# Performance work log

Measured on AMD Instinct MI355X. Metric: run time of the kernel, lower is better.

The kernel has to match this reference:

```python
import jax, jax.numpy as jnp
import numpy as np

DIM = 256
H = 8
D = 64
G = 64
INNER = H * D
SCALE = D ** -0.5


def setup_inputs() -> dict:
    key = jax.random.key(0)
    ks = jax.random.split(key, 12)
    B, N = 4, 16384
    x = jax.random.normal(ks[0], (B, N, DIM), dtype=jnp.float32)
    s = lambda fan_in: 1.0 / np.sqrt(fan_in)
    W_fx = jax.random.normal(ks[1], (DIM, INNER), dtype=jnp.float32) * s(DIM)
    b_fx = jnp.zeros((INNER,), dtype=jnp.float32)
    W_x = jax.random.normal(ks[2], (DIM, INNER), dtype=jnp.float32) * s(DIM)
    b_x = jnp.zeros((INNER,), dtype=jnp.float32)
    # orthogonal-ish init for slice projection
    A = jax.random.normal(ks[3], (G, D), dtype=jnp.float32)
    Q, _ = jnp.linalg.qr(A.T)  # (D, G) with orthonormal columns
    W_slice = Q[:, :G].astype(jnp.float32)  # (D, G)
    b_slice = jnp.zeros((G,), dtype=jnp.float32)
    W_q = jax.random.normal(ks[4], (D, D), dtype=jnp.float32) * s(D)
    W_k = jax.random.normal(ks[5], (D, D), dtype=jnp.float32) * s(D)
    W_v = jax.random.normal(ks[6], (D, D), dtype=jnp.float32) * s(D)
    W_out = jax.random.normal(ks[7], (INNER, DIM), dtype=jnp.float32) * s(INNER)
    b_out = jnp.zeros((DIM,), dtype=jnp.float32)
    temperature = jnp.ones((1, H, 1, 1), dtype=jnp.float32) * 0.5
    return {"x": x, "W_fx": W_fx, "b_fx": b_fx, "W_x": W_x, "b_x": b_x,
            "W_slice": W_slice, "b_slice": b_slice, "W_q": W_q, "W_k": W_k,
            "W_v": W_v, "W_out": W_out, "b_out": b_out, "temperature": temperature}


def reference(x, W_fx, b_fx, W_x, b_x, W_slice, b_slice, W_q, W_k, W_v, W_out, b_out, temperature):
    B, N, _ = x.shape
    # per-head projections: (B, H, N, D)
    fx_mid = (x @ W_fx + b_fx).reshape(B, N, H, D).transpose(0, 2, 1, 3)
    x_mid = (x @ W_x + b_x).reshape(B, N, H, D).transpose(0, 2, 1, 3)
    temp = jnp.clip(temperature, 0.1, 5.0)  # (1, H, 1, 1)
    # soft dispatch weights over G slices: (B, H, N, G)
    slice_weights = jax.nn.softmax((x_mid @ W_slice + b_slice) / temp, axis=-1)
    slice_norm = slice_weights.sum(axis=2)  # (B, H, G)
    # dispatch: pool N nodes into G slice tokens
    slice_token = jnp.einsum('bhnc,bhng->bhgc', fx_mid, slice_weights)
    slice_token = slice_token / (slice_norm[..., None] + 1e-5)
    # small attention among G slice tokens
    q = slice_token @ W_q
    k = slice_token @ W_k
    v = slice_token @ W_v
    attn = jax.nn.softmax(jnp.einsum('bhgc,bhkc->bhgk', q, k) * SCALE, axis=-1)
    out_slice = jnp.einsum('bhgk,bhkc->bhgc', attn, v)
    # combine: scatter slice tokens back to nodes
    out_x = jnp.einsum('bhgc,bhng->bhnc', out_slice, slice_weights)
    out_x = out_x.transpose(0, 2, 1, 3).reshape(B, N, INNER)
    return out_x @ W_out + b_out
```

## Files before the change

### kernel.cpp

```cpp
#include <hip/hip_runtime.h>
#include <hip/hip_bf16.h>


#define B_ 4
#define N_ 16384
#define DIM_ 256
#define H_ 8
#define D_ 64
#define G_ 64
#define INNER_ 512
#define SCALE_ 0.125f

typedef __attribute__((ext_vector_type(8))) short bf16x8;
typedef __attribute__((ext_vector_type(4))) float f32x4;
typedef unsigned short ushort_t;

#define MFMA(a, b, c) __builtin_amdgcn_mfma_f32_16x16x32_bf16((a), (b), (c), 0, 0, 0)

__device__ __forceinline__ ushort_t f2bf(float f) {
  unsigned u = __builtin_bit_cast(unsigned, f);
  u += 0x7FFFu + ((u >> 16) & 1u);
  return (ushort_t)(u >> 16);
}
__device__ __forceinline__ float bf2f(ushort_t h) {
  return __builtin_bit_cast(float, ((unsigned)h) << 16);
}
__device__ __forceinline__ uint2 pack4(f32x4 v) {
  uint2 r;
  r.x = (unsigned)f2bf(v[0]) | ((unsigned)f2bf(v[1]) << 16);
  r.y = (unsigned)f2bf(v[2]) | ((unsigned)f2bf(v[3]) << 16);
  return r;
}
__device__ __forceinline__ void gload16(const ushort_t* gsrc, char* ldst) {
  __builtin_amdgcn_global_load_lds(
      (const __attribute__((address_space(1))) unsigned int*)gsrc,
      (__attribute__((address_space(3))) unsigned int*)ldst, 16, 0, 0);
}

__global__ __launch_bounds__(256) void k0_prep(
    const float* __restrict__ x, const float* __restrict__ Wfx,
    const float* __restrict__ Wout, ushort_t* __restrict__ xh,
    ushort_t* __restrict__ xl, ushort_t* __restrict__ wfxt,
    ushort_t* __restrict__ wot) {
  const int bid = blockIdx.x;
  const int t = threadIdx.x;
  if (bid < 2048) {
    const float4* x4 = (const float4*)x;
    const int base = bid * 256 + t;
#pragma unroll
    for (int i = 0; i < 8; ++i) {
      const int idx = base + i * 524288;
      const float4 v = x4[idx];
      ushort_t h0 = f2bf(v.x), h1 = f2bf(v.y), h2 = f2bf(v.z), h3 = f2bf(v.w);
      uint2 hp, lp;
      hp.x = (unsigned)h0 | ((unsigned)h1 << 16);
      hp.y = (unsigned)h2 | ((unsigned)h3 << 16);
      lp.x = (unsigned)f2bf(v.x - bf2f(h0)) | ((unsigned)f2bf(v.y - bf2f(h1)) << 16);
      lp.y = (unsigned)f2bf(v.z - bf2f(h2)) | ((unsigned)f2bf(v.w - bf2f(h3)) << 16);
      *(uint2*)&xh[(size_t)idx * 4] = hp;
      *(uint2*)&xl[(size_t)idx * 4] = lp;
    }
  } else if (bid < 2560) {
    const int f = (bid - 2048) * 256 + t;
    const int k = f & 255, c = (f >> 8) & 63, h = f >> 14;
    wfxt[f] = f2bf(Wfx[(size_t)k * INNER_ + h * 64 + c]);
  } else {
    const int idx = (bid - 2560) * 256 + t;
    const int c = idx & 63, d = (idx >> 6) & 255, h = idx >> 14;
    wot[idx] = f2bf(Wout[(size_t)(h * 64 + c) * DIM_ + d]);
  }
}

__global__ __launch_bounds__(256) void k0b_comb(
    const float* __restrict__ Wx, const float* __restrict__ Wsl,
    const float* __restrict__ bx, const float* __restrict__ bsl,
    ushort_t* __restrict__ wcth, ushort_t* __restrict__ wctl,
    float* __restrict__ lbias) {
  __shared__ float wsl_s[4096];
  __shared__ float wx_s[64 * 65];
  const int h = blockIdx.x;
  const int t = threadIdx.x;
#pragma unroll
  for (int i = 0; i < 16; ++i) wsl_s[i * 256 + t] = Wsl[i * 256 + t];
  __syncthreads();
  if (t < 64) {
    float a = bsl[t];
    for (int dd = 0; dd < 64; ++dd) a += bx[h * 64 + dd] * wsl_s[dd * 64 + t];
    lbias[h * 64 + t] = a;
  }
  const int g = t & 63, ko = t >> 6;
  for (int kc = 0; kc < 4; ++kc) {
    __syncthreads();
#pragma unroll
    for (int i = 0; i < 16; ++i) {
      const int f = i * 256 + t;
      wx_s[(f >> 6) * 65 + (f & 63)] =
          Wx[(size_t)(kc * 64 + (f >> 6)) * INNER_ + h * 64 + (f & 63)];
    }
    __syncthreads();
    for (int kk = ko * 16; kk < ko * 16 + 16; ++kk) {
      float a = 0.f;
#pragma unroll 8
      for (int dd = 0; dd < 64; ++dd) a += wx_s[kk * 65 + dd] * wsl_s[dd * 64 + g];
      const int k = kc * 64 + kk;
      const ushort_t hi = f2bf(a);
      wcth[(size_t)(h * 64 + g) * 256 + k] = hi;
      wctl[(size_t)(h * 64 + g) * 256 + k] = f2bf(a - bf2f(hi));
    }
  }
}

__global__ __launch_bounds__(512, 4) void k1_proj(
    const ushort_t* __restrict__ xh, const ushort_t* __restrict__ xl,
    const ushort_t* __restrict__ wfxt, const ushort_t* __restrict__ wcth,
    const ushort_t* __restrict__ wctl, const float* __restrict__ bfx,
    const float* __restrict__ lbias, const float* __restrict__ temperature,
    ushort_t* __restrict__ w_buf, float* __restrict__ tok,
    float* __restrict__ nrm) {
  __shared__ __align__(16) char lds[57344];
  ushort_t* fxT = (ushort_t*)lds;
  ushort_t* wT = (ushort_t*)(lds + 17408);

  const int t = threadIdx.x;
  const int l = t & 63, w = t >> 6;
  const int l15 = l & 15, l4 = l >> 4;
  const int bid = blockIdx.x;
  const int tile = bid & 127, h = (bid >> 7) & 7, b = bid >> 10;
  const int n0 = tile * 128;
  const int bh = b * H_ + h;

  const ushort_t* xhg = xh + (size_t)(b * N_ + n0) * 256;
  const ushort_t* xlg = xl + (size_t)(b * N_ + n0) * 256;
  const ushort_t* wfg = wfxt + h * 16384;
  const ushort_t* wchg = wcth + h * 16384;
  const ushort_t* wclg = wctl + h * 16384;

  const int srow = l >> 2;
  const int schunk = (l & 3) * 8;

  f32x4 afx[4], alg[4];
#pragma unroll
  for (int cf = 0; cf < 4; ++cf) {
    const float bf_ = bfx[h * 64 + cf * 16 + l15];
    afx[cf][0] = bf_; afx[cf][1] = bf_; afx[cf][2] = bf_; afx[cf][3] = bf_;
    const float lb_ = lbias[h * 64 + cf * 16 + l15];
    alg[cf][0] = lb_; alg[cf][1] = lb_; alg[cf][2] = lb_; alg[cf][3] = lb_;
  }

#define STAGE(cur, ks)                                                          \
  {                                                                             \
    const int k0_ = (ks) * 32;                                                  \
    char* sb_ = lds + (cur) * 28672;                                            \
    gload16(xhg + (size_t)(w * 16 + srow) * 256 + k0_ + schunk, sb_ + w * 1024);\
    gload16(xlg + (size_t)(w * 16 + srow) * 256 + k0_ + schunk,                 \
            sb_ + 8192 + w * 1024);                                             \
    if (w < 4) {                                                                \
      gload16(wfg + (size_t)(w * 16 + srow) * 256 + k0_ + schunk,               \
              sb_ + 16384 + w * 1024);                                          \
      gload16(wclg + (size_t)(w * 16 + srow) * 256 + k0_ + schunk,              \
              sb_ + 24576 + w * 1024);                                          \
    } else {                                                                    \
      gload16(wchg + (size_t)((w - 4) * 16 + srow) * 256 + k0_ + schunk,        \
              sb_ + 20480 + (w - 4) * 1024);                                    \
    }                                                                           \
  }

  STAGE(0, 0);
  __syncthreads();
  int cur = 0;
  for (int ks = 0; ks < 8; ++ks) {
    if (ks < 7) STAGE(cur ^ 1, ks + 1);
    const char* sb = lds + cur * 28672;
    const int aoff = ((w * 16 + l15) * 32 + l4 * 8) * 2;
    const bf16x8 aXH = *(const bf16x8*)(sb + aoff);
    const bf16x8 aXL = *(const bf16x8*)(sb + 8192 + aoff);
    const int boff = (l15 * 32 + l4 * 8) * 2;
#pragma unroll
    for (int cf = 0; cf < 4; ++cf) {
      const bf16x8 bWF = *(const bf16x8*)(sb + 16384 + cf * 1024 + boff);
      afx[cf] = MFMA(aXH, bWF, afx[cf]);
      const bf16x8 bCH = *(const bf16x8*)(sb + 20480 + cf * 1024 + boff);
      alg[cf] = MFMA(aXH, bCH, alg[cf]);
      alg[cf] = MFMA(aXL, bCH, alg[cf]);
      const bf16x8 bCL = *(const bf16x8*)(sb + 24576 + cf * 1024 + boff);
      alg[cf] = MFMA(aXH, bCL, alg[cf]);
    }
    __syncthreads();
    cur ^= 1;
  }
#undef STAGE

#pragma unroll
  for (int cf = 0; cf < 4; ++cf)
    *(uint2*)&fxT[(cf * 16 + l15) * 136 + w * 16 + l4 * 4] = pack4(afx[cf]);

  float tmp = temperature[h];
  tmp = fminf(fmaxf(tmp, 0.1f), 5.0f);
  const float itemp = 1.0f / tmp;
  float wv[4][4];
#pragma unroll
  for (int r = 0; r < 4; ++r) {
    float m = fmaxf(fmaxf(alg[0][r], alg[1][r]), fmaxf(alg[2][r], alg[3][r])) * itemp;
    m = fmaxf(m, __shfl_xor(m, 1));
    m = fmaxf(m, __shfl_xor(m, 2));
    m = fmaxf(m, __shfl_xor(m, 4));
    m = fmaxf(m, __shfl_xor(m, 8));
    float s = 0.f;
#pragma unroll
    for (int gf = 0; gf < 4; ++gf) {
      wv[r][gf] = __expf(alg[gf][r] * itemp - m);
      s += wv[r][gf];
    }
    s += __shfl_xor(s, 1);
    s += __shfl_xor(s, 2);
    s += __shfl_xor(s, 4);
    s += __shfl_xor(s, 8);
    const float inv = 1.0f / s;
#pragma unroll
    for (int gf = 0; gf < 4; ++gf) wv[r][gf] *= inv;
  }

#pragma unroll
  for (int gf = 0; gf < 4; ++gf) {
    float pn = wv[0][gf] + wv[1][gf] + wv[2][gf] + wv[3][gf];
    pn += __shfl_xor(pn, 16);
    pn += __shfl_xor(pn, 32);
    if (l4 == 0) atomicAdd(&nrm[bh * 64 + gf * 16 + l15], pn);
  }

#pragma unroll
  for (int gf = 0; gf < 4; ++gf) {
    f32x4 v;
    v[0] = wv[0][gf]; v[1] = wv[1][gf]; v[2] = wv[2][gf]; v[3] = wv[3][gf];
    *(uint2*)&wT[(gf * 16 + l15) * 136 + w * 16 + l4 * 4] = pack4(v);
  }
  __syncthreads();

  {
    const int n = t >> 2, q = t & 3;
    unsigned up[8];
#pragma unroll
    for (int j = 0; j < 8; ++j) {
      const unsigned e0 = wT[(q * 16 + 2 * j) * 136 + n];
      const unsigned e1 = wT[(q * 16 + 2 * j + 1) * 136 + n];
      up[j] = e0 | (e1 << 16);
    }
    ushort_t* wg = w_buf + ((size_t)bh * N_ + n0 + n) * 64 + q * 16;
    *(int4*)&wg[0] = *(int4*)&up[0];
    *(int4*)&wg[8] = *(int4*)&up[4];
  }

  f32x4 ap[2];
  ap[0] = (f32x4)0.f;
  ap[1] = (f32x4)0.f;
  const int gf0 = (w * 2) >> 2, cf0 = (w * 2) & 3;
  const int gf1 = (w * 2 + 1) >> 2, cf1 = (w * 2 + 1) & 3;
#pragma unroll
  for (int ks = 0; ks < 4; ++ks) {
    const bf16x8 aW0 = *(const bf16x8*)&wT[(gf0 * 16 + l15) * 136 + ks * 32 + l4 * 8];
    const bf16x8 bF0 = *(const bf16x8*)&fxT[(cf0 * 16 + l15) * 136 + ks * 32 + l4 * 8];
    ap[0] = MFMA(aW0, bF0, ap[0]);
    const bf16x8 aW1 = *(const bf16x8*)&wT[(gf1 * 16 + l15) * 136 + ks * 32 + l4 * 8];
    const bf16x8 bF1 = *(const bf16x8*)&fxT[(cf1 * 16 + l15) * 136 + ks * 32 + l4 * 8];
    ap[1] = MFMA(aW1, bF1, ap[1]);
  }
#pragma unroll
  for (int u = 0; u < 2; ++u) {
    const int gf = (w * 2 + u) >> 2, cf = (w * 2 + u) & 3;
    const int c = cf * 16 + l15;
#pragma unroll
    for (int r = 0; r < 4; ++r) {
      const int g = gf * 16 + l4 * 4 + r;
      atomicAdd(&tok[((size_t)bh * 64 + g) * 64 + c], ap[u][r]);
    }
  }
}

__global__ __launch_bounds__(256) void k2_attn(
    const float* __restrict__ tok, const float* __restrict__ nrm,
    const float* __restrict__ Wq, const float* __restrict__ Wk,
    const float* __restrict__ Wv, ushort_t* __restrict__ outST) {
  __shared__ float st[64 * 65];
  __shared__ float qs[64 * 65];
  __shared__ float ks[64 * 68];
  __shared__ float vs[64 * 68];
  const int t = threadIdx.x;
  const int g = t & 63, qd = t >> 6;
  const int bh = blockIdx.x;

  const float rn = 1.0f / (nrm[bh * 64 + g] + 1e-5f);
  const float* tkr = tok + (size_t)bh * 4096 + g * 64;
#pragma unroll
  for (int dd = 0; dd < 16; ++dd) {
    const int d = qd * 16 + dd;
    st[g * 65 + d] = tkr[d] * rn;
  }
  __syncthreads();

  float qa[16], ka[16], va[16];
#pragma unroll
  for (int dd = 0; dd < 16; ++dd) { qa[dd] = 0.f; ka[dd] = 0.f; va[dd] = 0.f; }
  for (int c = 0; c < 64; ++c) {
    const float s = st[g * 65 + c];
    const float* wqp = Wq + c * 64 + qd * 16;
    const float* wkp = Wk + c * 64 + qd * 16;
    const float* wvp = Wv + c * 64 + qd * 16;
#pragma unroll
    for (int dd = 0; dd < 16; ++dd) {
      qa[dd] += s * wqp[dd];
      ka[dd] += s * wkp[dd];
      va[dd] += s * wvp[dd];
    }
  }
#pragma unroll
  for (int dd = 0; dd < 16; ++dd) {
    const int d = qd * 16 + dd;
    qs[g * 65 + d] = qa[dd];
    ks[g * 68 + d] = ka[dd];
    vs[g * 68 + d] = va[dd];
  }
  __syncthreads();

  float qr[64];
#pragma unroll
  for (int c = 0; c < 64; ++c) qr[c] = qs[g * 65 + c];
  float sc[16];
#pragma unroll
  for (int jj = 0; jj < 16; ++jj) {
    const int j = qd * 16 + jj;
    float a = 0.f;
#pragma unroll
    for (int c4 = 0; c4 < 16; ++c4) {
      const float4 kv = *(float4*)&ks[j * 68 + c4 * 4];
      a += qr[c4 * 4 + 0] * kv.x + qr[c4 * 4 + 1] * kv.y +
           qr[c4 * 4 + 2] * kv.z + qr[c4 * 4 + 3] * kv.w;
    }
    sc[jj] = a * SCALE_;
  }

  float* red = st;
  float m = sc[0];
#pragma unroll
  for (int jj = 1; jj < 16; ++jj) m = fmaxf(m, sc[jj]);
  red[qd * 64 + g] = m;
  __syncthreads();
  m = fmaxf(fmaxf(red[g], red[64 + g]), fmaxf(red[128 + g], red[192 + g]));
  float s = 0.f;
#pragma unroll
  for (int jj = 0; jj < 16; ++jj) {
    sc[jj] = __expf(sc[jj] - m);
    s += sc[jj];
  }
  red[256 + qd * 64 + g] = s;
  __syncthreads();
  s = red[256 + g] + red[256 + 64 + g] + red[256 + 128 + g] + red[256 + 192 + g];
  const float inv = 1.0f / s;
#pragma unroll
  for (int jj = 0; jj < 16; ++jj) qs[g * 65 + qd * 16 + jj] = sc[jj] * inv;
  __syncthreads();

  float pr[64];
#pragma unroll
  for (int c = 0; c < 64; ++c) pr[c] = qs[g * 65 + c];
  ushort_t* os = outST + (size_t)bh * 4096;
#pragma unroll
  for (int dd = 0; dd < 16; ++dd) {
    const int d = qd * 16 + dd;
    float o = 0.f;
#pragma unroll
    for (int j = 0; j < 64; ++j) o += pr[j] * vs[j * 68 + d];
    os[d * 64 + g] = f2bf(o);
  }
}

__global__ __launch_bounds__(512, 1) void k3_out(
    const ushort_t* __restrict__ w_buf, const ushort_t* __restrict__ outST,
    const ushort_t* __restrict__ wot, const float* __restrict__ bout,
    float* __restrict__ out) {
  __shared__ ushort_t a_lds[128 * 72];
  __shared__ ushort_t wot_lds[256 * 72];
  const int t = threadIdx.x;
  const int l = t & 63, w = t >> 6;
  const int l15 = l & 15, l4 = l >> 4;
  const int bid = blockIdx.x;
  const int tile = bid & 127, b = bid >> 7;
  const int n0 = tile * 128;

  f32x4 acc[16];
#pragma unroll
  for (int df = 0; df < 16; ++df)
#pragma unroll
    for (int r = 0; r < 4; ++r) acc[df][r] = bout[df * 16 + l4 * 4 + r];

  for (int h = 0; h < H_; ++h) {
    const int bh = b * H_ + h;
    __syncthreads();
#pragma unroll
    for (int i = 0; i < 4; ++i) {
      const int idx = t + 512 * i;
      const int row = idx >> 3, q = idx & 7;
      *(int4*)&wot_lds[row * 72 + q * 8] =
          *(const int4*)&wot[((size_t)h * 256 + row) * 64 + q * 8];
    }
    f32x4 as_[4];
#pragma unroll
    for (int cf = 0; cf < 4; ++cf) as_[cf] = (f32x4)0.f;
#pragma unroll
    for (int ks = 0; ks < 2; ++ks) {
      const bf16x8 bW = *(const bf16x8*)&w_buf[((size_t)bh * N_ + n0 + w * 16 + l15) * 64 +
                                               ks * 32 + l4 * 8];
#pragma unroll
      for (int cf = 0; cf < 4; ++cf) {
        const bf16x8 aS = *(const bf16x8*)&outST[(size_t)bh * 4096 + (cf * 16 + l15) * 64 +
                                                 ks * 32 + l4 * 8];
        as_[cf] = MFMA(aS, bW, as_[cf]);
      }
    }
#pragma unroll
    for (int cf = 0; cf < 4; ++cf)
      *(uint2*)&a_lds[(w * 16 + l15) * 72 + cf * 16 + l4 * 4] = pack4(as_[cf]);
    __syncthreads();
#pragma unroll
    for (int ks = 0; ks < 2; ++ks) {
      const bf16x8 bA = *(const bf16x8*)&a_lds[(w * 16 + l15) * 72 + ks * 32 + l4 * 8];
#pragma unroll
      for (int df = 0; df < 16; ++df) {
        const bf16x8 aW = *(const bf16x8*)&wot_lds[(df * 16 + l15) * 72 + ks * 32 + l4 * 8];
        acc[df] = MFMA(aW, bA, acc[df]);
      }
    }
  }

  const int n = n0 + w * 16 + l15;
  float* og = out + ((size_t)b * N_ + n) * DIM_;
#pragma unroll
  for (int df = 0; df < 16; ++df) {
    float4 v;
    v.x = acc[df][0]; v.y = acc[df][1]; v.z = acc[df][2]; v.w = acc[df][3];
    *(float4*)&og[df * 16 + l4 * 4] = v;
  }
}

extern "C" void kernel_launch(void* const* d_in, const int* in_sizes, int n_in,
                              void* d_out, int out_size, void* d_ws, size_t ws_size,
                              hipStream_t stream) {
  const float* x = (const float*)d_in[0];
  const float* Wfx = (const float*)d_in[1];
  const float* bfx = (const float*)d_in[2];
  const float* Wx = (const float*)d_in[3];
  const float* bx = (const float*)d_in[4];
  const float* Wsl = (const float*)d_in[5];
  const float* bsl = (const float*)d_in[6];
  const float* Wq = (const float*)d_in[7];
  const float* Wk = (const float*)d_in[8];
  const float* Wv = (const float*)d_in[9];
  const float* Wout = (const float*)d_in[10];
  const float* bout = (const float*)d_in[11];
  const float* temp = (const float*)d_in[12];

  char* ws = (char*)d_ws;
  ushort_t* w_buf = (ushort_t*)ws;
  ushort_t* xh = (ushort_t*)(ws + 67108864);
  ushort_t* xl = (ushort_t*)(ws + 100663296);
  ushort_t* wfxt = (ushort_t*)(ws + 134217728);
  ushort_t* wcth = (ushort_t*)(ws + 134479872);
  ushort_t* wctl = (ushort_t*)(ws + 134742016);
  ushort_t* wot = (ushort_t*)(ws + 135004160);
  ushort_t* outST = (ushort_t*)(ws + 135266304);
  float* tok = (float*)(ws + 135528448);
  float* nrm = (float*)(ws + 136052736);
  float* lbias = (float*)(ws + 136060928);

  hipMemsetAsync(tok, 0, 524288 + 8192, stream);

  k0_prep<<<dim3(3072), dim3(256), 0, stream>>>(x, Wfx, Wout, xh, xl, wfxt, wot);
  k0b_comb<<<dim3(8), dim3(256), 0, stream>>>(Wx, Wsl, bx, bsl, wcth, wctl, lbias);
  k1_proj<<<dim3(B_ * H_ * (N_ / 128)), dim3(512), 0, stream>>>(
      xh, xl, wfxt, wcth, wctl, bfx, lbias, temp, w_buf, tok, nrm);
  k2_attn<<<dim3(B_ * H_), dim3(256), 0, stream>>>(tok, nrm, Wq, Wk, Wv, outST);
  k3_out<<<dim3(B_ * (N_ / 128)), dim3(512), 0, stream>>>(w_buf, outST, wot,
                                                          bout, (float*)d_out);
}
```

Measured before the change: 514.7 us.

## Double k1 tile to 256 rows, keep weights resident in swizzled LDS, stream x directly

The projection kernel now handles 256 nodes per block instead of 128. It loads the whole per-head weight slice (fx, combined hi and lo) into LDS once, using an XOR-swizzled layout, and reads the x operands straight from global memory into registers instead of double-buffering them through LDS. This halves the block count and the tok/nrm atomic traffic per node, and removes the per-k-step barriers. The cost is more LDS per block (96KB), lower occupancy bounds and unhidden global-load latency for x.

```diff
diff --git a/kernel.cpp b/kernel.cpp
--- a/kernel.cpp
+++ b/kernel.cpp
@@ -10,6 +10,7 @@
 #define G_ 64
 #define INNER_ 512
 #define SCALE_ 0.125f
+#define TILE_ 256
 
 typedef __attribute__((ext_vector_type(8))) short bf16x8;
 typedef __attribute__((ext_vector_type(4))) float f32x4;
@@ -110,144 +111,156 @@
   }
 }
 
-__global__ __launch_bounds__(512, 4) void k1_proj(
+__global__ __launch_bounds__(512, 2) void k1_proj(
     const ushort_t* __restrict__ xh, const ushort_t* __restrict__ xl,
     const ushort_t* __restrict__ wfxt, const ushort_t* __restrict__ wcth,
     const ushort_t* __restrict__ wctl, const float* __restrict__ bfx,
     const float* __restrict__ lbias, const float* __restrict__ temperature,
     ushort_t* __restrict__ w_buf, float* __restrict__ tok,
     float* __restrict__ nrm) {
-  __shared__ __align__(16) char lds[57344];
+  __shared__ __align__(16) char lds[98304];
   ushort_t* fxT = (ushort_t*)lds;
-  ushort_t* wT = (ushort_t*)(lds + 17408);
+  ushort_t* wT = (ushort_t*)(lds + 33792);
 
   const int t = threadIdx.x;
   const int l = t & 63, w = t >> 6;
   const int l15 = l & 15, l4 = l >> 4;
   const int bid = blockIdx.x;
-  const int tile = bid & 127, h = (bid >> 7) & 7, b = bid >> 10;
-  const int n0 = tile * 128;
+  const int tile = bid & 63, h = (bid >> 6) & 7, b = bid >> 9;
+  const int n0 = tile * TILE_;
   const int bh = b * H_ + h;
 
-  const ushort_t* xhg = xh + (size_t)(b * N_ + n0) * 256;
-  const ushort_t* xlg = xl + (size_t)(b * N_ + n0) * 256;
+  const ushort_t* xhg = xh + ((size_t)b * N_ + n0) * 256;
+  const ushort_t* xlg = xl + ((size_t)b * N_ + n0) * 256;
   const ushort_t* wfg = wfxt + h * 16384;
   const ushort_t* wchg = wcth + h * 16384;
   const ushort_t* wclg = wctl + h * 16384;
 
-  const int srow = l >> 2;
-  const int schunk = (l & 3) * 8;
-
-  f32x4 afx[4], alg[4];
+#pragma unroll
+  for (int it = 0; it < 12; ++it) {
+    const int ci = it * 512 + t;
+    const int m = ci >> 11;
+    const int cm = ci & 2047;
+    const int row = cm >> 5, c = cm & 31;
+    const int sc = c ^ (row & 7);
+    const ushort_t* src = (m == 0) ? wfg : (m == 1) ? wchg : wclg;
+    gload16(src + row * 256 + sc * 8, lds + ci * 16);
+  }
+  __syncthreads();
+
+  f32x4 afx[2][4], alg[2][4];
 #pragma unroll
   for (int cf = 0; cf < 4; ++cf) {
     const float bf_ = bfx[h * 64 + cf * 16 + l15];
-    afx[cf][0] = bf_; afx[cf][1] = bf_; afx[cf][2] = bf_; afx[cf][3] = bf_;
     const float lb_ = lbias[h * 64 + cf * 16 + l15];
-    alg[cf][0] = lb_; alg[cf][1] = lb_; alg[cf][2] = lb_; alg[cf][3] = lb_;
-  }
-
-#define STAGE(cur, ks)                                                          \
-  {                                                                             \
-    const int k0_ = (ks) * 32;                                                  \
-    char* sb_ = lds + (cur) * 28672;                                            \
-    gload16(xhg + (size_t)(w * 16 + srow) * 256 + k0_ + schunk, sb_ + w * 1024);\
-    gload16(xlg + (size_t)(w * 16 + srow) * 256 + k0_ + schunk,                 \
-            sb_ + 8192 + w * 1024);                                             \
-    if (w < 4) {                                                                \
-      gload16(wfg + (size_t)(w * 16 + srow) * 256 + k0_ + schunk,               \
-              sb_ + 16384 + w * 1024);                                          \
-      gload16(wclg + (size_t)(w * 16 + srow) * 256 + k0_ + schunk,              \
-              sb_ + 24576 + w * 1024);                                          \
-    } else {                                                                    \
-      gload16(wchg + (size_t)((w - 4) * 16 + srow) * 256 + k0_ + schunk,        \
-              sb_ + 20480 + (w - 4) * 1024);                                    \
-    }                                                                           \
-  }
-
-  STAGE(0, 0);
-  __syncthreads();
-  int cur = 0;
+#pragma unroll
+    for (int rf = 0; rf < 2; ++rf) {
+      afx[rf][cf][0] = bf_; afx[rf][cf][1] = bf_; afx[rf][cf][2] = bf_; afx[rf][cf][3] = bf_;
+      alg[rf][cf][0] = lb_; alg[rf][cf][1] = lb_; alg[rf][cf][2] = lb_; alg[rf][cf][3] = lb_;
+    }
+  }
+
+  const int arow = (w * 32 + l15) * 256 + l4 * 8;
+  const int key = l15 & 7;
+
+#pragma unroll
   for (int ks = 0; ks < 8; ++ks) {
-    if (ks < 7) STAGE(cur ^ 1, ks + 1);
-    const char* sb = lds + cur * 28672;
-    const int aoff = ((w * 16 + l15) * 32 + l4 * 8) * 2;
-    const bf16x8 aXH = *(const bf16x8*)(sb + aoff);
-    const bf16x8 aXL = *(const bf16x8*)(sb + 8192 + aoff);
-    const int boff = (l15 * 32 + l4 * 8) * 2;
+    const int kh = ks * 32;
+    const bf16x8 xh0 = *(const bf16x8*)&xhg[arow + kh];
+    const bf16x8 xh1 = *(const bf16x8*)&xhg[arow + 4096 + kh];
+    const bf16x8 xl0 = *(const bf16x8*)&xlg[arow + kh];
+    const bf16x8 xl1 = *(const bf16x8*)&xlg[arow + 4096 + kh];
 #pragma unroll
     for (int cf = 0; cf < 4; ++cf) {
-      const bf16x8 bWF = *(const bf16x8*)(sb + 16384 + cf * 1024 + boff);
-      afx[cf] = MFMA(aXH, bWF, afx[cf]);
-      const bf16x8 bCH = *(const bf16x8*)(sb + 20480 + cf * 1024 + boff);
-      alg[cf] = MFMA(aXH, bCH, alg[cf]);
-      alg[cf] = MFMA(aXL, bCH, alg[cf]);
-      const bf16x8 bCL = *(const bf16x8*)(sb + 24576 + cf * 1024 + boff);
-      alg[cf] = MFMA(aXH, bCL, alg[cf]);
-    }
-    __syncthreads();
-    cur ^= 1;
-  }
-#undef STAGE
-
-#pragma unroll
-  for (int cf = 0; cf < 4; ++cf)
-    *(uint2*)&fxT[(cf * 16 + l15) * 136 + w * 16 + l4 * 4] = pack4(afx[cf]);
+      const int coff = (cf * 16 + l15) * 512 + (((ks * 4 + l4) ^ key) * 16);
+      const bf16x8 bF = *(const bf16x8*)(lds + coff);
+      const bf16x8 bH = *(const bf16x8*)(lds + 32768 + coff);
+      const bf16x8 bL = *(const bf16x8*)(lds + 65536 + coff);
+      afx[0][cf] = MFMA(xh0, bF, afx[0][cf]);
+      afx[1][cf] = MFMA(xh1, bF, afx[1][cf]);
+      alg[0][cf] = MFMA(xh0, bH, alg[0][cf]);
+      alg[0][cf] = MFMA(xl0, bH, alg[0][cf]);
+      alg[0][cf] = MFMA(xh0, bL, alg[0][cf]);
+      alg[1][cf] = MFMA(xh1, bH, alg[1][cf]);
+      alg[1][cf] = MFMA(xl1, bH, alg[1][cf]);
+      alg[1][cf] = MFMA(xh1, bL, alg[1][cf]);
+    }
+  }
+  __syncthreads();
+
+#pragma unroll
+  for (int rf = 0; rf < 2; ++rf)
+#pragma unroll
+    for (int cf = 0; cf < 4; ++cf)
+      *(uint2*)&fxT[(cf * 16 + l15) * 264 + w * 32 + rf * 16 + l4 * 4] =
+          pack4(afx[rf][cf]);
 
   float tmp = temperature[h];
   tmp = fminf(fmaxf(tmp, 0.1f), 5.0f);
   const float itemp = 1.0f / tmp;
-  float wv[4][4];
-#pragma unroll
-  for (int r = 0; r < 4; ++r) {
-    float m = fmaxf(fmaxf(alg[0][r], alg[1][r]), fmaxf(alg[2][r], alg[3][r])) * itemp;
-    m = fmaxf(m, __shfl_xor(m, 1));
-    m = fmaxf(m, __shfl_xor(m, 2));
-    m = fmaxf(m, __shfl_xor(m, 4));
-    m = fmaxf(m, __shfl_xor(m, 8));
-    float s = 0.f;
-#pragma unroll
-    for (int gf = 0; gf < 4; ++gf) {
-      wv[r][gf] = __expf(alg[gf][r] * itemp - m);
-      s += wv[r][gf];
-    }
-    s += __shfl_xor(s, 1);
-    s += __shfl_xor(s, 2);
-    s += __shfl_xor(s, 4);
-    s += __shfl_xor(s, 8);
-    const float inv = 1.0f / s;
-#pragma unroll
-    for (int gf = 0; gf < 4; ++gf) wv[r][gf] *= inv;
-  }
+  float wv[2][4][4];
+#pragma unroll
+  for (int rf = 0; rf < 2; ++rf)
+#pragma unroll
+    for (int r = 0; r < 4; ++r) {
+      float m = fmaxf(fmaxf(alg[rf][0][r], alg[rf][1][r]),
+                      fmaxf(alg[rf][2][r], alg[rf][3][r])) * itemp;
+      m = fmaxf(m, __shfl_xor(m, 1));
+      m = fmaxf(m, __shfl_xor(m, 2));
+      m = fmaxf(m, __shfl_xor(m, 4));
+      m = fmaxf(m, __shfl_xor(m, 8));
+      float s = 0.f;
+#pragma unroll
+      for (int gf = 0; gf < 4; ++gf) {
+        wv[rf][r][gf] = __expf(alg[rf][gf][r] * itemp - m);
+        s += wv[rf][r][gf];
+      }
+      s += __shfl_xor(s, 1);
+      s += __shfl_xor(s, 2);
+      s += __shfl_xor(s, 4);
+      s += __shfl_xor(s, 8);
+      const float inv = 1.0f / s;
+#pragma unroll
+      for (int gf = 0; gf < 4; ++gf) wv[rf][r][gf] *= inv;
+    }
 
 #pragma unroll
   for (int gf = 0; gf < 4; ++gf) {
-    float pn = wv[0][gf] + wv[1][gf] + wv[2][gf] + wv[3][gf];
+    float pn = 0.f;
+#pragma unroll
+    for (int rf = 0; rf < 2; ++rf)
+#pragma unroll
+      for (int r = 0; r < 4; ++r) pn += wv[rf][r][gf];
     pn += __shfl_xor(pn, 16);
     pn += __shfl_xor(pn, 32);
     if (l4 == 0) atomicAdd(&nrm[bh * 64 + gf * 16 + l15], pn);
   }
 
 #pragma unroll
-  for (int gf = 0; gf < 4; ++gf) {
-    f32x4 v;
-    v[0] = wv[0][gf]; v[1] = wv[1][gf]; v[2] = wv[2][gf]; v[3] = wv[3][gf];
-    *(uint2*)&wT[(gf * 16 + l15) * 136 + w * 16 + l4 * 4] = pack4(v);
-  }
+  for (int rf = 0; rf < 2; ++rf)
+#pragma unroll
+    for (int gf = 0; gf < 4; ++gf) {
+      f32x4 v;
+      v[0] = wv[rf][0][gf]; v[1] = wv[rf][1][gf];
+      v[2] = wv[rf][2][gf]; v[3] = wv[rf][3][gf];
+      *(uint2*)&wT[(gf * 16 + l15) * 264 + w * 32 + rf * 16 + l4 * 4] = pack4(v);
+    }
   __syncthreads();
 
   {
-    const int n = t >> 2, q = t & 3;
-    unsigned up[8];
-#pragma unroll
-    for (int j = 0; j < 8; ++j) {
-      const unsigned e0 = wT[(q * 16 + 2 * j) * 136 + n];
-      const unsigned e1 = wT[(q * 16 + 2 * j + 1) * 136 + n];
+    const int n = t >> 1, q = t & 1;
+    unsigned up[16];
+#pragma unroll
+    for (int j = 0; j < 16; ++j) {
+      const unsigned e0 = wT[(q * 32 + 2 * j) * 264 + n];
+      const unsigned e1 = wT[(q * 32 + 2 * j + 1) * 264 + n];
       up[j] = e0 | (e1 << 16);
     }
-    ushort_t* wg = w_buf + ((size_t)bh * N_ + n0 + n) * 64 + q * 16;
+    ushort_t* wg = w_buf + ((size_t)bh * N_ + n0 + n) * 64 + q * 32;
     *(int4*)&wg[0] = *(int4*)&up[0];
     *(int4*)&wg[8] = *(int4*)&up[4];
+    *(int4*)&wg[16] = *(int4*)&up[8];
+    *(int4*)&wg[24] = *(int4*)&up[12];
   }
 
   f32x4 ap[2];
@@ -256,12 +269,12 @@
   const int gf0 = (w * 2) >> 2, cf0 = (w * 2) & 3;
   const int gf1 = (w * 2 + 1) >> 2, cf1 = (w * 2 + 1) & 3;
 #pragma unroll
-  for (int ks = 0; ks < 4; ++ks) {
-    const bf16x8 aW0 = *(const bf16x8*)&wT[(gf0 * 16 + l15) * 136 + ks * 32 + l4 * 8];
-    const bf16x8 bF0 = *(const bf16x8*)&fxT[(cf0 * 16 + l15) * 136 + ks * 32 + l4 * 8];
+  for (int ks = 0; ks < 8; ++ks) {
+    const bf16x8 aW0 = *(const bf16x8*)&wT[(gf0 * 16 + l15) * 264 + ks * 32 + l4 * 8];
+    const bf16x8 bF0 = *(const bf16x8*)&fxT[(cf0 * 16 + l15) * 264 + ks * 32 + l4 * 8];
     ap[0] = MFMA(aW0, bF0, ap[0]);
-    const bf16x8 aW1 = *(const bf16x8*)&wT[(gf1 * 16 + l15) * 136 + ks * 32 + l4 * 8];
-    const bf16x8 bF1 = *(const bf16x8*)&fxT[(cf1 * 16 + l15) * 136 + ks * 32 + l4 * 8];
+    const bf16x8 aW1 = *(const bf16x8*)&wT[(gf1 * 16 + l15) * 264 + ks * 32 + l4 * 8];
+    const bf16x8 bF1 = *(const bf16x8*)&fxT[(cf1 * 16 + l15) * 264 + ks * 32 + l4 * 8];
     ap[1] = MFMA(aW1, bF1, ap[1]);
   }
 #pragma unroll
@@ -475,7 +488,7 @@
 
   k0_prep<<<dim3(3072), dim3(256), 0, stream>>>(x, Wfx, Wout, xh, xl, wfxt, wot);
   k0b_comb<<<dim3(8), dim3(256), 0, stream>>>(Wx, Wsl, bx, bsl, wcth, wctl, lbias);
-  k1_proj<<<dim3(B_ * H_ * (N_ / 128)), dim3(512), 0, stream>>>(
+  k1_proj<<<dim3(B_ * H_ * (N_ / TILE_)), dim3(512), 0, stream>>>(
       xh, xl, wfxt, wcth, wctl, bfx, lbias, temp, w_buf, tok, nrm);
   k2_attn<<<dim3(B_ * H_), dim3(256), 0, stream>>>(tok, nrm, Wq, Wk, Wv, outST);
   k3_out<<<dim3(B_ * (N_ / 128)), dim3(512), 0, stream>>>(w_buf, outST, wot,
```

Result: faster. 470.2 us (-8.6%).
